# Optimization experiments

Measured on AMD Instinct MI355X. Metric: run time of the kernel, lower is better.

The kernel has to match this reference:

```python
import jax, jax.numpy as jnp
import numpy as np

HS = 4096
NIN = 17   # RFSIZE*RFSIZE + ADDINPUT + NBACTIONS = 9 + 4 + 4
NACT = 4


def setup_inputs() -> dict:
    key = jax.random.key(0)
    ks = jax.random.split(key, 10)
    return {
        "inputs": jax.random.normal(ks[0], (1, NIN), jnp.float32),
        "hidden": jax.random.normal(ks[1], (1, HS), jnp.float32) * 0.1,
        "hebb": jnp.zeros((HS, HS), jnp.float32),
        "et": jnp.zeros((HS, HS), jnp.float32),
        "pw": jnp.zeros((HS, HS), jnp.float32),
        # i2h Linear(17 -> hs)
        "i2h_w": jax.random.normal(ks[2], (HS, NIN), jnp.float32) * (1.0 / np.sqrt(NIN)),
        "i2h_b": jax.random.normal(ks[3], (HS,), jnp.float32) * 0.01,
        # plastic recurrent params: 0.01 * rand, eta = 0.01 * ones(1)
        "w": 0.01 * jax.random.uniform(ks[4], (HS, HS), jnp.float32),
        "alpha": 0.01 * jax.random.uniform(ks[5], (HS, HS), jnp.float32),
        "eta": 0.01 * jnp.ones((1,), jnp.float32),
        # output heads
        "h2o_w": jax.random.normal(ks[6], (NACT, HS), jnp.float32) * (1.0 / np.sqrt(HS)),
        "h2o_b": jax.random.normal(ks[7], (NACT,), jnp.float32) * 0.01,
        "h2v_w": jax.random.normal(ks[8], (1, HS), jnp.float32) * (1.0 / np.sqrt(HS)),
        "h2v_b": jax.random.normal(ks[9], (1,), jnp.float32) * 0.01,
    }


def reference(inputs, hidden, hebb, et, pw,
              i2h_w, i2h_b, w, alpha, eta,
              h2o_w, h2o_b, h2v_w, h2v_b):
    # type='plastic', rule='hebb', clp=0, addpw=0
    # hactiv = tanh(i2h(inputs) + hidden @ (w + alpha * hebb))
    pre = inputs @ i2h_w.T + i2h_b + hidden @ (w + alpha * hebb)  # [1, HS]
    hactiv = jnp.tanh(pre)
    activout = hactiv @ h2o_w.T + h2o_b   # [1, NBACTIONS]
    valueout = hactiv @ h2v_w.T + h2v_b   # [1, 1]
    # deltahebb = outer(hidden[0], hactiv[0])  (batch 1, matches torch.bmm(...)[0])
    deltahebb = hidden[0][:, None] * hactiv[0][None, :]  # [HS, HS]
    hebb_new = (1.0 - eta) * hebb + eta * deltahebb       # eta shape (1,) broadcasts
    # hidden <- hactiv; et, pw untouched for this type
    return activout, valueout, hactiv, hebb_new, et, pw
```

## Files before the change

### kernel.cpp

```cpp
#include <hip/hip_runtime.h>
#include <math.h>

#define HS 4096
#define NIN 17
#define ROW_CHUNKS 512
#define ROWS_PER_CHUNK (HS / ROW_CHUNKS)

typedef float vfloat4 __attribute__((ext_vector_type(4)));

__device__ __forceinline__ vfloat4 ntload4(const vfloat4* p) {
  return __builtin_nontemporal_load(p);
}
__device__ __forceinline__ float ntloadf(const float* p) {
  return __builtin_nontemporal_load(p);
}
__device__ __forceinline__ void ntstoref(float* p, float v) {
  __builtin_nontemporal_store(v, p);
}

__global__ __launch_bounds__(256) void matvec_copy_k(
    const float* __restrict__ hidden, const float* __restrict__ w,
    const float* __restrict__ alpha, const float* __restrict__ hebb,
    const float* __restrict__ et, const float* __restrict__ pw,
    float* __restrict__ partial, float* __restrict__ out_et,
    float* __restrict__ out_pw) {
  const int j4 = blockIdx.x * blockDim.x + threadIdx.x;
  const int row0 = blockIdx.y * ROWS_PER_CHUNK;
  const size_t base = (size_t)row0 * (HS / 4) + j4;
  const vfloat4* wp = reinterpret_cast<const vfloat4*>(w) + base;
  const vfloat4* ap = reinterpret_cast<const vfloat4*>(alpha) + base;
  const vfloat4* bp = reinterpret_cast<const vfloat4*>(hebb) + base;
  vfloat4 acc = (vfloat4)(0.f);
#pragma unroll
  for (int r = 0; r < ROWS_PER_CHUNK; ++r) {
    const float h = hidden[row0 + r];
    const vfloat4 wv = ntload4(wp + (size_t)r * (HS / 4));
    const vfloat4 av = ntload4(ap + (size_t)r * (HS / 4));
    const vfloat4 bv = bp[(size_t)r * (HS / 4)];
#pragma unroll
    for (int c = 0; c < 4; ++c)
      acc[c] = fmaf(h, fmaf(av[c], bv[c], wv[c]), acc[c]);
  }
  reinterpret_cast<vfloat4*>(partial)[(size_t)blockIdx.y * (HS / 4) + j4] = acc;

  const size_t cbase = ((size_t)blockIdx.y * gridDim.x + blockIdx.x) * 8192 + threadIdx.x;
#pragma unroll
  for (int i = 0; i < 32; ++i) {
    const size_t t = cbase + (size_t)i * 256;
    ntstoref(out_et + t, ntloadf(et + t));
    ntstoref(out_pw + t, ntloadf(pw + t));
  }
}

__global__ __launch_bounds__(64) void finalize_k(
    const float* __restrict__ partial, const float* __restrict__ inputs,
    const float* __restrict__ i2h_w, const float* __restrict__ i2h_b,
    float* __restrict__ out_hactiv) {
  const int j = blockIdx.x;
  const int lane = threadIdx.x;
  float s = 0.f;
#pragma unroll
  for (int i = 0; i < ROW_CHUNKS / 64; ++i)
    s += partial[(size_t)(lane + 64 * i) * HS + j];
  if (lane < NIN) s = fmaf(inputs[lane], i2h_w[j * NIN + lane], s);
#pragma unroll
  for (int off = 32; off > 0; off >>= 1) s += __shfl_down(s, off, 64);
  if (lane == 0) out_hactiv[j] = tanhf(s + i2h_b[j]);
}

__global__ __launch_bounds__(256) void heads_k(
    const float* __restrict__ hactiv, const float* __restrict__ h2o_w,
    const float* __restrict__ h2o_b, const float* __restrict__ h2v_w,
    const float* __restrict__ h2v_b, float* __restrict__ out) {
  const int r = blockIdx.x;
  const float* wrow = (r < 4) ? (h2o_w + (size_t)r * HS) : h2v_w;
  float s = 0.f;
  for (int j = threadIdx.x; j < HS; j += 256) s = fmaf(hactiv[j], wrow[j], s);
  __shared__ float red[256];
  red[threadIdx.x] = s;
  __syncthreads();
  for (int off = 128; off > 0; off >>= 1) {
    if (threadIdx.x < off) red[threadIdx.x] += red[threadIdx.x + off];
    __syncthreads();
  }
  if (threadIdx.x == 0) out[r] = red[0] + ((r < 4) ? h2o_b[r] : h2v_b[0]);
}

__global__ __launch_bounds__(256) void hebb_k(
    const float* __restrict__ hebb, const float* __restrict__ hidden,
    const float* __restrict__ hactiv, const float* __restrict__ eta,
    float* __restrict__ out_hebb) {
  const unsigned NSQ = (unsigned)HS * HS;
  const unsigned stride = gridDim.x * blockDim.x;
  const float e = eta[0];
  const float one_m_e = 1.f - e;
  for (unsigned t = blockIdx.x * blockDim.x + threadIdx.x; t < NSQ; t += stride) {
    const float hi = hidden[t >> 12];
    const float ha = hactiv[t & (HS - 1)];
    ntstoref(out_hebb + t, fmaf(one_m_e, hebb[t], e * hi * ha));
  }
}

extern "C" void kernel_launch(void* const* d_in, const int* in_sizes, int n_in,
                              void* d_out, int out_size, void* d_ws, size_t ws_size,
                              hipStream_t stream) {
  const float* inputs = (const float*)d_in[0];
  const float* hidden = (const float*)d_in[1];
  const float* hebb   = (const float*)d_in[2];
  const float* et     = (const float*)d_in[3];
  const float* pw     = (const float*)d_in[4];
  const float* i2h_w  = (const float*)d_in[5];
  const float* i2h_b  = (const float*)d_in[6];
  const float* w      = (const float*)d_in[7];
  const float* alpha  = (const float*)d_in[8];
  const float* eta    = (const float*)d_in[9];
  const float* h2o_w  = (const float*)d_in[10];
  const float* h2o_b  = (const float*)d_in[11];
  const float* h2v_w  = (const float*)d_in[12];
  const float* h2v_b  = (const float*)d_in[13];

  float* out = (float*)d_out;
  const size_t NSQ = (size_t)HS * HS;
  float* out_heads  = out;
  float* out_hactiv = out + 5;
  float* out_hebb   = out + 5 + HS;
  float* out_et     = out_hebb + NSQ;
  float* out_pw     = out_et + NSQ;

  const size_t need = (size_t)ROW_CHUNKS * HS * sizeof(float);
  float* partial = (ws_size >= need) ? (float*)d_ws
                                     : (out_hebb + 3 );

  hipLaunchKernelGGL(matvec_copy_k, dim3(HS / 4 / 256, ROW_CHUNKS), dim3(256),
                     0, stream, hidden, w, alpha, hebb, et, pw,
                     partial, out_et, out_pw);
  hipLaunchKernelGGL(finalize_k, dim3(HS), dim3(64), 0, stream,
                     partial, inputs, i2h_w, i2h_b, out_hactiv);
  hipLaunchKernelGGL(heads_k, dim3(5), dim3(256), 0, stream,
                     out_hactiv, h2o_w, h2o_b, h2v_w, h2v_b, out_heads);
  hipLaunchKernelGGL(hebb_k, dim3(2048), dim3(256), 0, stream,
                     hebb, hidden, out_hactiv, eta, out_hebb);
}
```

Baseline: 481.8 us.

## Move et/pw copy into elementwise kernel, batch matvec loads, drop nontemporal hints

The et/pw copy moves out of the matvec kernel and into a fused elementwise kernel alongside the hebb update, using a fixed 8-iteration unrolled layout instead of a grid-stride loop. The matvec kernel now issues all row loads up front into register arrays and sets a launch-bounds occupancy hint. Nontemporal load/store hints are removed everywhere. The aim is to raise memory-level parallelism and balance traffic, at the cost of register pressure and the loss of cache-bypass behaviour.

```diff
diff --git a/kernel.cpp b/kernel.cpp
--- a/kernel.cpp
+++ b/kernel.cpp
@@ -8,48 +8,33 @@
 
 typedef float vfloat4 __attribute__((ext_vector_type(4)));
 
-__device__ __forceinline__ vfloat4 ntload4(const vfloat4* p) {
-  return __builtin_nontemporal_load(p);
-}
-__device__ __forceinline__ float ntloadf(const float* p) {
-  return __builtin_nontemporal_load(p);
-}
-__device__ __forceinline__ void ntstoref(float* p, float v) {
-  __builtin_nontemporal_store(v, p);
-}
-
-__global__ __launch_bounds__(256) void matvec_copy_k(
+__global__ __launch_bounds__(256, 4) void matvec_k(
     const float* __restrict__ hidden, const float* __restrict__ w,
     const float* __restrict__ alpha, const float* __restrict__ hebb,
-    const float* __restrict__ et, const float* __restrict__ pw,
-    float* __restrict__ partial, float* __restrict__ out_et,
-    float* __restrict__ out_pw) {
+    float* __restrict__ partial) {
   const int j4 = blockIdx.x * blockDim.x + threadIdx.x;
   const int row0 = blockIdx.y * ROWS_PER_CHUNK;
   const size_t base = (size_t)row0 * (HS / 4) + j4;
   const vfloat4* wp = reinterpret_cast<const vfloat4*>(w) + base;
   const vfloat4* ap = reinterpret_cast<const vfloat4*>(alpha) + base;
   const vfloat4* bp = reinterpret_cast<const vfloat4*>(hebb) + base;
+
+  vfloat4 wv[ROWS_PER_CHUNK], av[ROWS_PER_CHUNK], bv[ROWS_PER_CHUNK];
+#pragma unroll
+  for (int r = 0; r < ROWS_PER_CHUNK; ++r) {
+    wv[r] = wp[(size_t)r * (HS / 4)];
+    av[r] = ap[(size_t)r * (HS / 4)];
+    bv[r] = bp[(size_t)r * (HS / 4)];
+  }
   vfloat4 acc = (vfloat4)(0.f);
 #pragma unroll
   for (int r = 0; r < ROWS_PER_CHUNK; ++r) {
     const float h = hidden[row0 + r];
-    const vfloat4 wv = ntload4(wp + (size_t)r * (HS / 4));
-    const vfloat4 av = ntload4(ap + (size_t)r * (HS / 4));
-    const vfloat4 bv = bp[(size_t)r * (HS / 4)];
 #pragma unroll
     for (int c = 0; c < 4; ++c)
-      acc[c] = fmaf(h, fmaf(av[c], bv[c], wv[c]), acc[c]);
+      acc[c] = fmaf(h, fmaf(av[r][c], bv[r][c], wv[r][c]), acc[c]);
   }
   reinterpret_cast<vfloat4*>(partial)[(size_t)blockIdx.y * (HS / 4) + j4] = acc;
-
-  const size_t cbase = ((size_t)blockIdx.y * gridDim.x + blockIdx.x) * 8192 + threadIdx.x;
-#pragma unroll
-  for (int i = 0; i < 32; ++i) {
-    const size_t t = cbase + (size_t)i * 256;
-    ntstoref(out_et + t, ntloadf(et + t));
-    ntstoref(out_pw + t, ntloadf(pw + t));
-  }
 }
 
 __global__ __launch_bounds__(64) void finalize_k(
@@ -86,18 +71,32 @@
   if (threadIdx.x == 0) out[r] = red[0] + ((r < 4) ? h2o_b[r] : h2v_b[0]);
 }
 
-__global__ __launch_bounds__(256) void hebb_k(
+#define EW_THREADS (1u << 21)
+__global__ __launch_bounds__(256) void elementwise_k(
     const float* __restrict__ hebb, const float* __restrict__ hidden,
     const float* __restrict__ hactiv, const float* __restrict__ eta,
-    float* __restrict__ out_hebb) {
-  const unsigned NSQ = (unsigned)HS * HS;
-  const unsigned stride = gridDim.x * blockDim.x;
+    const float* __restrict__ et, const float* __restrict__ pw,
+    float* __restrict__ out_hebb, float* __restrict__ out_et,
+    float* __restrict__ out_pw) {
+  const unsigned tid = blockIdx.x * blockDim.x + threadIdx.x;
   const float e = eta[0];
-  const float one_m_e = 1.f - e;
-  for (unsigned t = blockIdx.x * blockDim.x + threadIdx.x; t < NSQ; t += stride) {
+  const float ome = 1.f - e;
+#pragma unroll
+  for (int i = 0; i < 8; ++i) {
+    const unsigned t = tid + (unsigned)i * EW_THREADS;
     const float hi = hidden[t >> 12];
     const float ha = hactiv[t & (HS - 1)];
-    ntstoref(out_hebb + t, fmaf(one_m_e, hebb[t], e * hi * ha));
+    out_hebb[t] = fmaf(ome, hebb[t], e * hi * ha);
+  }
+#pragma unroll
+  for (int i = 0; i < 8; ++i) {
+    const unsigned t = tid + (unsigned)i * EW_THREADS;
+    out_et[t] = et[t];
+  }
+#pragma unroll
+  for (int i = 0; i < 8; ++i) {
+    const unsigned t = tid + (unsigned)i * EW_THREADS;
+    out_pw[t] = pw[t];
   }
 }
 
@@ -131,13 +130,13 @@
   float* partial = (ws_size >= need) ? (float*)d_ws
                                      : (out_hebb + 3 );
 
-  hipLaunchKernelGGL(matvec_copy_k, dim3(HS / 4 / 256, ROW_CHUNKS), dim3(256),
-                     0, stream, hidden, w, alpha, hebb, et, pw,
-                     partial, out_et, out_pw);
+  hipLaunchKernelGGL(matvec_k, dim3(HS / 4 / 256, ROW_CHUNKS), dim3(256),
+                     0, stream, hidden, w, alpha, hebb, partial);
   hipLaunchKernelGGL(finalize_k, dim3(HS), dim3(64), 0, stream,
                      partial, inputs, i2h_w, i2h_b, out_hactiv);
   hipLaunchKernelGGL(heads_k, dim3(5), dim3(256), 0, stream,
                      out_hactiv, h2o_w, h2o_b, h2v_w, h2v_b, out_heads);
-  hipLaunchKernelGGL(hebb_k, dim3(2048), dim3(256), 0, stream,
-                     hebb, hidden, out_hactiv, eta, out_hebb);
+  hipLaunchKernelGGL(elementwise_k, dim3(EW_THREADS / 256), dim3(256), 0, stream,
+                     hebb, hidden, out_hactiv, eta, et, pw,
+                     out_hebb, out_et, out_pw);
 }
```

After: 494.1 us. +2.5%, slower.

## Fuse all stages into one cooperative persistent kernel with grid syncs

Applied to the files above, without the earlier changes.

Merges the matvec-plus-copy, reduction, heads and hebb-update kernels into one cooperative kernel of 512 blocks that separates the phases with grid.sync, and keeps a three-kernel fallback. It reduces the partial-sum chunks from 512 to 128, which shrinks the partial buffer and the reduction traffic, and it replaces the nontemporal loads and stores with ordinary ones. The goal is to remove launch gaps and tail effects between stages, and the hebb reread may now hit cache. The risks are grid-sync cost, lower parallelism in the matvec phase, and losing the nontemporal streaming hints on roughly 400MB of traffic.

```diff
diff --git a/kernel.cpp b/kernel.cpp
--- a/kernel.cpp
+++ b/kernel.cpp
@@ -1,104 +1,151 @@
 #include <hip/hip_runtime.h>
+#include <hip/hip_cooperative_groups.h>
 #include <math.h>
+
+namespace cg = cooperative_groups;
 
 #define HS 4096
 #define NIN 17
-#define ROW_CHUNKS 512
-#define ROWS_PER_CHUNK (HS / ROW_CHUNKS)
+#define NBLK 512
+#define CHUNKS 128
+#define ROWS 32
+#define PER_BLK (HS * HS / NBLK)
 
 typedef float vfloat4 __attribute__((ext_vector_type(4)));
 
-__device__ __forceinline__ vfloat4 ntload4(const vfloat4* p) {
-  return __builtin_nontemporal_load(p);
-}
-__device__ __forceinline__ float ntloadf(const float* p) {
-  return __builtin_nontemporal_load(p);
-}
-__device__ __forceinline__ void ntstoref(float* p, float v) {
-  __builtin_nontemporal_store(v, p);
+
+__device__ __forceinline__ void phaseA_body(
+    int b, int tid, const float* __restrict__ hidden,
+    const float* __restrict__ w, const float* __restrict__ alpha,
+    const float* __restrict__ hebb, const float* __restrict__ et,
+    const float* __restrict__ pw, float* __restrict__ partial,
+    float* __restrict__ out_et, float* __restrict__ out_pw) {
+  const int colg = b & 3;
+  const int chunk = b >> 2;
+  const int j4 = colg * 256 + tid;
+  const int row0 = chunk * ROWS;
+  const size_t base = (size_t)row0 * (HS / 4) + j4;
+  const vfloat4* wp = reinterpret_cast<const vfloat4*>(w) + base;
+  const vfloat4* ap = reinterpret_cast<const vfloat4*>(alpha) + base;
+  const vfloat4* bp = reinterpret_cast<const vfloat4*>(hebb) + base;
+  vfloat4 acc = (vfloat4)(0.f);
+#pragma unroll 8
+  for (int r = 0; r < ROWS; ++r) {
+    const float h = hidden[row0 + r];
+    const vfloat4 wv = wp[(size_t)r * (HS / 4)];
+    const vfloat4 av = ap[(size_t)r * (HS / 4)];
+    const vfloat4 bv = bp[(size_t)r * (HS / 4)];
+#pragma unroll
+    for (int c = 0; c < 4; ++c)
+      acc[c] = fmaf(h, fmaf(av[c], bv[c], wv[c]), acc[c]);
+  }
+  reinterpret_cast<vfloat4*>(partial)[(size_t)chunk * (HS / 4) + j4] = acc;
+
+  const size_t cb = (size_t)b * PER_BLK + tid;
+#pragma unroll 8
+  for (int i = 0; i < PER_BLK / 256; ++i) {
+    const size_t t = cb + (size_t)i * 256;
+    out_et[t] = et[t];
+    out_pw[t] = pw[t];
+  }
 }
 
-__global__ __launch_bounds__(256) void matvec_copy_k(
+__device__ __forceinline__ void phaseB_body(
+    int b, int tid, const float* __restrict__ partial,
+    const float* __restrict__ inputs, const float* __restrict__ i2h_w,
+    const float* __restrict__ i2h_b, float* __restrict__ out_hactiv) {
+  const int g = tid >> 6, lane = tid & 63;
+#pragma unroll
+  for (int c = 0; c < 2; ++c) {
+    const int j = (b * 4 + g) + 2048 * c;
+    float s = 0.f;
+#pragma unroll
+    for (int i = 0; i < CHUNKS / 64; ++i)
+      s += partial[(size_t)(lane + 64 * i) * HS + j];
+    if (lane < NIN) s = fmaf(inputs[lane], i2h_w[j * NIN + lane], s);
+#pragma unroll
+    for (int off = 32; off > 0; off >>= 1) s += __shfl_down(s, off, 64);
+    if (lane == 0) out_hactiv[j] = tanhf(s + i2h_b[j]);
+  }
+}
+
+__device__ __forceinline__ void phaseC_body(
+    int b, int tid, const float* __restrict__ hidden,
+    const float* __restrict__ hebb, const float* __restrict__ eta,
+    const float* __restrict__ h2o_w, const float* __restrict__ h2o_b,
+    const float* __restrict__ h2v_w, const float* __restrict__ h2v_b,
+    const float* __restrict__ hactiv, float* __restrict__ out_heads,
+    float* __restrict__ out_hebb) {
+  if (b < 5 && tid < 64) {
+    const float* wrow = (b < 4) ? (h2o_w + (size_t)b * HS) : h2v_w;
+    float s = 0.f;
+    for (int i = tid; i < HS; i += 64) s = fmaf(hactiv[i], wrow[i], s);
+#pragma unroll
+    for (int off = 32; off > 0; off >>= 1) s += __shfl_down(s, off, 64);
+    if (tid == 0) out_heads[b] = s + ((b < 4) ? h2o_b[b] : h2v_b[0]);
+  }
+  const float e = eta[0];
+  const float ome = 1.f - e;
+  const size_t cb = (size_t)b * PER_BLK + tid;
+#pragma unroll 8
+  for (int i = 0; i < PER_BLK / 256; ++i) {
+    const size_t t = cb + (size_t)i * 256;
+    const float hi = hidden[t >> 12];
+    const float ha = hactiv[t & (HS - 1)];
+    out_hebb[t] = fmaf(ome, hebb[t], e * hi * ha);
+  }
+}
+
+
+__global__ __launch_bounds__(256, 2) void fused_k(
+    const float* __restrict__ inputs, const float* __restrict__ hidden,
+    const float* __restrict__ hebb, const float* __restrict__ et,
+    const float* __restrict__ pw, const float* __restrict__ i2h_w,
+    const float* __restrict__ i2h_b, const float* __restrict__ w,
+    const float* __restrict__ alpha, const float* __restrict__ eta,
+    const float* __restrict__ h2o_w, const float* __restrict__ h2o_b,
+    const float* __restrict__ h2v_w, const float* __restrict__ h2v_b,
+    float* __restrict__ partial, float* __restrict__ out_heads,
+    float* __restrict__ out_hactiv, float* __restrict__ out_hebb,
+    float* __restrict__ out_et, float* __restrict__ out_pw) {
+  cg::grid_group grid = cg::this_grid();
+  phaseA_body(blockIdx.x, threadIdx.x, hidden, w, alpha, hebb, et, pw,
+              partial, out_et, out_pw);
+  grid.sync();
+  phaseB_body(blockIdx.x, threadIdx.x, partial, inputs, i2h_w, i2h_b,
+              out_hactiv);
+  grid.sync();
+  phaseC_body(blockIdx.x, threadIdx.x, hidden, hebb, eta, h2o_w, h2o_b,
+              h2v_w, h2v_b, out_hactiv, out_heads, out_hebb);
+}
+
+
+__global__ __launch_bounds__(256, 2) void phaseA_k(
     const float* __restrict__ hidden, const float* __restrict__ w,
     const float* __restrict__ alpha, const float* __restrict__ hebb,
     const float* __restrict__ et, const float* __restrict__ pw,
     float* __restrict__ partial, float* __restrict__ out_et,
     float* __restrict__ out_pw) {
-  const int j4 = blockIdx.x * blockDim.x + threadIdx.x;
-  const int row0 = blockIdx.y * ROWS_PER_CHUNK;
-  const size_t base = (size_t)row0 * (HS / 4) + j4;
-  const vfloat4* wp = reinterpret_cast<const vfloat4*>(w) + base;
-  const vfloat4* ap = reinterpret_cast<const vfloat4*>(alpha) + base;
-  const vfloat4* bp = reinterpret_cast<const vfloat4*>(hebb) + base;
-  vfloat4 acc = (vfloat4)(0.f);
-#pragma unroll
-  for (int r = 0; r < ROWS_PER_CHUNK; ++r) {
-    const float h = hidden[row0 + r];
-    const vfloat4 wv = ntload4(wp + (size_t)r * (HS / 4));
-    const vfloat4 av = ntload4(ap + (size_t)r * (HS / 4));
-    const vfloat4 bv = bp[(size_t)r * (HS / 4)];
-#pragma unroll
-    for (int c = 0; c < 4; ++c)
-      acc[c] = fmaf(h, fmaf(av[c], bv[c], wv[c]), acc[c]);
-  }
-  reinterpret_cast<vfloat4*>(partial)[(size_t)blockIdx.y * (HS / 4) + j4] = acc;
-
-  const size_t cbase = ((size_t)blockIdx.y * gridDim.x + blockIdx.x) * 8192 + threadIdx.x;
-#pragma unroll
-  for (int i = 0; i < 32; ++i) {
-    const size_t t = cbase + (size_t)i * 256;
-    ntstoref(out_et + t, ntloadf(et + t));
-    ntstoref(out_pw + t, ntloadf(pw + t));
-  }
+  phaseA_body(blockIdx.x, threadIdx.x, hidden, w, alpha, hebb, et, pw,
+              partial, out_et, out_pw);
 }
 
-__global__ __launch_bounds__(64) void finalize_k(
+__global__ __launch_bounds__(256, 2) void phaseB_k(
     const float* __restrict__ partial, const float* __restrict__ inputs,
     const float* __restrict__ i2h_w, const float* __restrict__ i2h_b,
     float* __restrict__ out_hactiv) {
-  const int j = blockIdx.x;
-  const int lane = threadIdx.x;
-  float s = 0.f;
-#pragma unroll
-  for (int i = 0; i < ROW_CHUNKS / 64; ++i)
-    s += partial[(size_t)(lane + 64 * i) * HS + j];
-  if (lane < NIN) s = fmaf(inputs[lane], i2h_w[j * NIN + lane], s);
-#pragma unroll
-  for (int off = 32; off > 0; off >>= 1) s += __shfl_down(s, off, 64);
-  if (lane == 0) out_hactiv[j] = tanhf(s + i2h_b[j]);
+  phaseB_body(blockIdx.x, threadIdx.x, partial, inputs, i2h_w, i2h_b,
+              out_hactiv);
 }
 
-__global__ __launch_bounds__(256) void heads_k(
-    const float* __restrict__ hactiv, const float* __restrict__ h2o_w,
+__global__ __launch_bounds__(256, 2) void phaseC_k(
+    const float* __restrict__ hidden, const float* __restrict__ hebb,
+    const float* __restrict__ eta, const float* __restrict__ h2o_w,
     const float* __restrict__ h2o_b, const float* __restrict__ h2v_w,
-    const float* __restrict__ h2v_b, float* __restrict__ out) {
-  const int r = blockIdx.x;
-  const float* wrow = (r < 4) ? (h2o_w + (size_t)r * HS) : h2v_w;
-  float s = 0.f;
-  for (int j = threadIdx.x; j < HS; j += 256) s = fmaf(hactiv[j], wrow[j], s);
-  __shared__ float red[256];
-  red[threadIdx.x] = s;
-  __syncthreads();
-  for (int off = 128; off > 0; off >>= 1) {
-    if (threadIdx.x < off) red[threadIdx.x] += red[threadIdx.x + off];
-    __syncthreads();
-  }
-  if (threadIdx.x == 0) out[r] = red[0] + ((r < 4) ? h2o_b[r] : h2v_b[0]);
-}
-
-__global__ __launch_bounds__(256) void hebb_k(
-    const float* __restrict__ hebb, const float* __restrict__ hidden,
-    const float* __restrict__ hactiv, const float* __restrict__ eta,
-    float* __restrict__ out_hebb) {
-  const unsigned NSQ = (unsigned)HS * HS;
-  const unsigned stride = gridDim.x * blockDim.x;
-  const float e = eta[0];
-  const float one_m_e = 1.f - e;
-  for (unsigned t = blockIdx.x * blockDim.x + threadIdx.x; t < NSQ; t += stride) {
-    const float hi = hidden[t >> 12];
-    const float ha = hactiv[t & (HS - 1)];
-    ntstoref(out_hebb + t, fmaf(one_m_e, hebb[t], e * hi * ha));
-  }
+    const float* __restrict__ h2v_b, const float* __restrict__ hactiv,
+    float* __restrict__ out_heads, float* __restrict__ out_hebb) {
+  phaseC_body(blockIdx.x, threadIdx.x, hidden, hebb, eta, h2o_w, h2o_b,
+              h2v_w, h2v_b, hactiv, out_heads, out_hebb);
 }
 
 extern "C" void kernel_launch(void* const* d_in, const int* in_sizes, int n_in,
@@ -127,17 +174,26 @@
   float* out_et     = out_hebb + NSQ;
   float* out_pw     = out_et + NSQ;
 
-  const size_t need = (size_t)ROW_CHUNKS * HS * sizeof(float);
+  const size_t need = (size_t)CHUNKS * HS * sizeof(float);
   float* partial = (ws_size >= need) ? (float*)d_ws
                                      : (out_hebb + 3 );
 
-  hipLaunchKernelGGL(matvec_copy_k, dim3(HS / 4 / 256, ROW_CHUNKS), dim3(256),
-                     0, stream, hidden, w, alpha, hebb, et, pw,
-                     partial, out_et, out_pw);
-  hipLaunchKernelGGL(finalize_k, dim3(HS), dim3(64), 0, stream,
-                     partial, inputs, i2h_w, i2h_b, out_hactiv);
-  hipLaunchKernelGGL(heads_k, dim3(5), dim3(256), 0, stream,
-                     out_hactiv, h2o_w, h2o_b, h2v_w, h2v_b, out_heads);
-  hipLaunchKernelGGL(hebb_k, dim3(2048), dim3(256), 0, stream,
-                     hebb, hidden, out_hactiv, eta, out_hebb);
+  void* args[] = {
+      (void*)&inputs, (void*)&hidden, (void*)&hebb, (void*)&et, (void*)&pw,
+      (void*)&i2h_w, (void*)&i2h_b, (void*)&w, (void*)&alpha, (void*)&eta,
+      (void*)&h2o_w, (void*)&h2o_b, (void*)&h2v_w, (void*)&h2v_b,
+      (void*)&partial, (void*)&out_heads, (void*)&out_hactiv,
+      (void*)&out_hebb, (void*)&out_et, (void*)&out_pw};
+  hipError_t err = hipLaunchCooperativeKernel(
+      (const void*)fused_k, dim3(NBLK), dim3(256), args, 0, stream);
+  if (err != hipSuccess) {
+    (void)hipGetLastError();
+    hipLaunchKernelGGL(phaseA_k, dim3(NBLK), dim3(256), 0, stream,
+                       hidden, w, alpha, hebb, et, pw, partial, out_et, out_pw);
+    hipLaunchKernelGGL(phaseB_k, dim3(NBLK), dim3(256), 0, stream,
+                       partial, inputs, i2h_w, i2h_b, out_hactiv);
+    hipLaunchKernelGGL(phaseC_k, dim3(NBLK), dim3(256), 0, stream,
+                       hidden, hebb, eta, h2o_w, h2o_b, h2v_w, h2v_b,
+                       out_hactiv, out_heads, out_hebb);
+  }
 }
```

Result: slower. 647.0 us (+34.3%).
